# Kernel tuning notes

Measured on AMD Instinct MI355X. Metric: run time of the kernel, lower is better.

The kernel has to match this reference:

```python
import jax, jax.numpy as jnp
import numpy as np

B, V, K, DIN, H, DH, OBS, HID = 2048, 3, 32, 256, 8, 64, 128, 256
REP = H * DH
EPS = 1e-6


def _ln(x, g, b):
    mu = x.mean(-1, keepdims=True)
    var = ((x - mu) ** 2).mean(-1, keepdims=True)
    return (x - mu) * jax.lax.rsqrt(var + 1e-5) * g + b


def setup_inputs() -> dict:
    key = jax.random.key(0)
    ks = iter(jax.random.split(key, 32))
    nrm = lambda shape, s=0.05: jax.random.normal(next(ks), shape, jnp.float32) * s
    return {
        'x_anchor': jax.random.normal(next(ks), (B, V, DIN), jnp.float32),
        'x_neighbors': jax.random.normal(next(ks), (B, V, K, DIN), jnp.float32),
        'edge_weights': jax.random.uniform(next(ks), (B, V, K), jnp.float32),
        'g': jax.random.normal(next(ks), (B, OBS), jnp.float32),
        'aW': nrm((V, DIN, REP)), 'ab': jnp.zeros((V, REP)), 'ag': jnp.ones((V, REP)), 'abeta': jnp.zeros((V, REP)),
        'nW': nrm((V, DIN, REP)), 'nb': jnp.zeros((V, REP)), 'ng': jnp.ones((V, REP)), 'nbeta': jnp.zeros((V, REP)),
        'Wq': nrm((V, H, DH, DH)), 'Wk': nrm((V, H, DH, DH)), 'Wv': nrm((V, H, DH, DH)), 'Wo': nrm((V, H, DH, DH)),
        'geom_log_scale': jnp.zeros((V, H)),
        'cWq': nrm((H, DH, DH)), 'cWk': nrm((H, DH, DH)), 'cWv': nrm((H, DH, DH)), 'cWo': nrm((H, DH, DH)),
        'rW1': nrm((OBS, HID)), 'rb1': jnp.zeros((HID,)),
        'rW2': nrm((HID, HID)), 'rb2': jnp.zeros((HID,)),
        'vW': nrm((HID, H * V)), 'vb': jnp.zeros((H * V,)),
        'mW': nrm((HID, H)), 'mb': jnp.zeros((H,)),
        'gW': nrm((HID, H)), 'gb': jnp.zeros((H,)),
    }


def reference(x_anchor, x_neighbors, edge_weights, g, aW, ab, ag, abeta, nW, nb, ng, nbeta,
              Wq, Wk, Wv, Wo, geom_log_scale, cWq, cWk, cWv, cWo,
              rW1, rb1, rW2, rb2, vW, vb, mW, mb, gW, gb):
    # --- per-view encoders (vectorized over V with a leading v axis) ---
    ha = _ln(jnp.einsum('bvi,vio->bvo', x_anchor, aW) + ab, ag, abeta).reshape(B, V, H, DH)
    hn = _ln(jnp.einsum('bvki,vio->bvko', x_neighbors, nW) + nb[:, None, :],
             ng[:, None, :], nbeta[:, None, :]).reshape(B, V, K, H, DH)
    q = jnp.einsum('bvhd,vhde->bvhe', ha, Wq)
    k = jnp.einsum('bvkhd,vhde->bvkhe', hn, Wk)
    vv = jnp.einsum('bvkhd,vhde->bvkhe', hn, Wv)
    sc = jnp.einsum('bvhd,bvkhd->bvhk', q, k) / np.sqrt(DH).astype(np.float32)
    geom = jax.nn.softplus(geom_log_scale)  # [V,H]
    sc = sc + geom[None, :, :, None] * jnp.log(edge_weights[:, :, None, :] + EPS)
    attn = jax.nn.softmax(sc, axis=-1)
    ho = jnp.einsum('bvhk,bvkhd->bvhd', attn, vv)
    ho = jnp.einsum('bvhd,vhde->bvhe', ho, Wo) + ha  # residual
    view_tokens = jnp.transpose(ho, (0, 2, 1, 3))  # [B,H,V,Dh]
    # --- router ---
    hid = jax.nn.gelu(jnp.dot(g, rW1) + rb1, approximate=False)
    hid = jax.nn.gelu(jnp.dot(hid, rW2) + rb2, approximate=False)
    pi = jax.nn.softmax((jnp.dot(hid, vW) + vb).reshape(B, H, V), axis=-1)
    beta = jax.nn.sigmoid((jnp.dot(hid, mW) + mb)[..., None])  # [B,H,1]
    gate = jax.nn.softmax(jnp.dot(hid, gW) + gb, axis=-1)      # [B,H]
    # --- pi-weighted mixture + cross-view interaction with log-pi prior ---
    mix = jnp.einsum('bhv,bhvd->bhd', pi, view_tokens)
    qc = jnp.einsum('bhd,hde->bhe', mix, cWq)
    kc = jnp.einsum('bhvd,hde->bhve', view_tokens, cWk)
    vc = jnp.einsum('bhvd,hde->bhve', view_tokens, cWv)
    s2 = jnp.einsum('bhd,bhvd->bhv', qc, kc) / np.sqrt(DH).astype(np.float32) + jnp.log(pi + EPS)
    a2 = jax.nn.softmax(s2, axis=-1)
    cr = jnp.einsum('bhv,bhvd->bhd', a2, vc)
    cr = jnp.einsum('bhd,hde->bhe', cr, cWo)
    # mode blend + head gating; head_repr kept unflattened [B,H,Dh]
    return gate[..., None] * (beta * cr + (1.0 - beta) * mix)
```

## Files before the change

### kernel.cpp

```cpp
#include <hip/hip_runtime.h>

#define B_   2048
#define V_   3
#define K_   32
#define DIN_ 256
#define H_   8
#define DH_  64
#define REP_ 512

typedef unsigned short u16;
typedef unsigned int   u32;
typedef __bf16 bf8 __attribute__((ext_vector_type(8)));
typedef float  f4  __attribute__((ext_vector_type(4)));

static __device__ __forceinline__ u16 f2bf(float f) {
  union { float f; u32 i; } x; x.f = f;
  u32 r = (x.i + 0x7FFFu + ((x.i >> 16) & 1u)) >> 16;
  return (u16)r;
}
static __device__ __forceinline__ float bf2f(u16 u) {
  union { u32 i; float f; } x; x.i = ((u32)u) << 16;
  return x.f;
}
static __device__ __forceinline__ float bflo(u32 q) {
  union { u32 i; float f; } x; x.i = q << 16; return x.f;
}
static __device__ __forceinline__ float bfhi(u32 q) {
  union { u32 i; float f; } x; x.i = q & 0xffff0000u; return x.f;
}

static __device__ __forceinline__ void gl2lds16(const u16* g, u16* l) {
  __builtin_amdgcn_global_load_lds(
      (const __attribute__((address_space(1))) unsigned int*)(g),
      (__attribute__((address_space(3))) unsigned int*)(l), 16, 0, 0);
}

__global__ __launch_bounds__(256) void k0_prep(
    const float* __restrict__ nW, const float* __restrict__ aW,
    const float* __restrict__ Wv,
    u16* __restrict__ nWt, u16* __restrict__ aWt,
    u16* __restrict__ Wvt)
{
  int id = blockIdx.x * 256 + threadIdx.x;
  if (id < 393216) {
    int v  = id / 131072, r  = id % 131072;
    int kt = r / 16384,   r2 = r % 16384;
    int n  = r2 >> 5;
    int s  = (r2 >> 3) & 3;
    int m  = r2 & 7;
    int c  = s ^ ((n >> 1) & 3);
    int k  = kt * 32 + c * 8 + m;
    int src = (v * 256 + k) * 512 + n;
    nWt[id] = f2bf(nW[src]);
    aWt[id] = f2bf(aW[src]);
  } else {
    int j = id - 393216;
    int vh = j / 4096, r = j % 4096;
    int e = r / 64, d = r % 64;
    int src = (vh * 64 + d) * 64 + e;
    Wvt[j] = f2bf(Wv[src]);
  }
}

__global__ __launch_bounds__(256) void k0_wqk(
    const float* __restrict__ Wq, const float* __restrict__ Wk,
    float* __restrict__ Wqk)
{
  int vh = blockIdx.x, t = threadIdx.x;
  __shared__ float wq[4096], wkT[4096];
  #pragma unroll
  for (int i = 0; i < 16; ++i) {
    int idx = i * 256 + t;
    wq[idx] = Wq[(long)vh * 4096 + idx];
    int e = idx >> 6, c = idx & 63;
    wkT[c * 64 + e] = Wk[(long)vh * 4096 + e * 64 + c];
  }
  __syncthreads();
  int d = t >> 2, e0 = (t & 3) * 16;
  float acc[16];
  #pragma unroll
  for (int j = 0; j < 16; ++j) acc[j] = 0.f;
  for (int c = 0; c < 64; ++c) {
    float a = wq[d * 64 + c];
    const float* wr = &wkT[c * 64 + e0];
    #pragma unroll
    for (int j = 0; j < 16; ++j) acc[j] += a * wr[j];
  }
  #pragma unroll
  for (int j = 0; j < 16; ++j) Wqk[(long)vh * 4096 + d * 64 + e0 + j] = acc[j];
}

__global__ __launch_bounds__(256) void k_tq(
    const float* __restrict__ ha, const float* __restrict__ Wqk,
    float* __restrict__ tB)
{
  __shared__ float hs[512];
  int bv = blockIdx.x, t = threadIdx.x;
  int v = bv % 3;
  hs[t]       = ha[(long)bv * 512 + t];
  hs[256 + t] = ha[(long)bv * 512 + 256 + t];
  __syncthreads();
  int h = t >> 5, e0 = (t & 31) * 2;
  const float* wq = Wqk + ((long)v * 8 + h) * 4096 + e0;
  const float* hv = &hs[h * 64];
  float a0 = 0.f, a1 = 0.f;
  #pragma unroll 4
  for (int d = 0; d < 64; ++d) {
    float x = hv[d];
    float2 wv = *(const float2*)&wq[d * 64];
    a0 += x * wv.x;
    a1 += x * wv.y;
  }
  tB[(long)bv * 512 + h * 64 + e0]     = a0 * 0.125f;
  tB[(long)bv * 512 + h * 64 + e0 + 1] = a1 * 0.125f;
}

union K1Smem {
  struct { u16 A[64 * 256]; u16 B[16384]; } p;
  u16 S[64 * 512];
};

__global__ __launch_bounds__(512, 4) void k1_gemm_ln(
    const float* __restrict__ X,
    const u16*   __restrict__ Wt,
    const float* __restrict__ bias,
    const float* __restrict__ gamma,
    const float* __restrict__ betap,
    u16*   __restrict__ hn,
    float* __restrict__ ha,
    int mode, int b0, int Bc)
{
  __shared__ K1Smem sm;
  const int v = blockIdx.y, blk = blockIdx.x, t = threadIdx.x;
  const int w = t >> 6, l = t & 63, lm = l & 15, lg = l >> 4;
  const int wm = w & 1, wn = w >> 1;

  float bcol[8];
  #pragma unroll
  for (int tn = 0; tn < 8; ++tn) bcol[tn] = bias[v * 512 + wn * 128 + tn * 16 + lm];

  {
    int row = t >> 3;
    int cbase = (t & 7) * 32;
    long grow;
    if (mode == 0) { int b = b0 + blk * 2 + (row >> 5); grow = ((long)(b * 3 + v) * 32 + (row & 31)) * 256; }
    else           { int b = blk * 64 + row;            grow = (long)(b * 3 + v) * 256; }
    const float4* src = (const float4*)(X + grow + cbase);
    int sw = row & 7;
    #pragma unroll
    for (int j = 0; j < 8; ++j) {
      float4 f = src[j];
      int col = cbase + j * 4;
      int c = col >> 3, m = col & 7;
      ushort4 u;
      u.x = f2bf(f.x); u.y = f2bf(f.y); u.z = f2bf(f.z); u.w = f2bf(f.w);
      *(ushort4*)&sm.p.A[row * 256 + ((c ^ sw) << 3) + m] = u;
    }
  }

  f4 acc[2][8];
  #pragma unroll
  for (int i = 0; i < 2; ++i)
    #pragma unroll
    for (int j = 0; j < 8; ++j) { f4 z = {0.f, 0.f, 0.f, 0.f}; acc[i][j] = z; }

  const u16* Wbase = Wt + (long)v * 8 * 16384;
  for (int kt = 0; kt < 8; ++kt) {
    __syncthreads();
    {
      const u16* gp = Wbase + (long)kt * 16384 + t * 8;
      u16* lp = &sm.p.B[t * 8];
      #pragma unroll
      for (int r = 0; r < 4; ++r) gl2lds16(gp + r * 4096, lp + r * 4096);
    }
    __syncthreads();
    bf8 af[2];
    #pragma unroll
    for (int tm = 0; tm < 2; ++tm) {
      int row = wm * 32 + tm * 16 + lm;
      int c = kt * 4 + lg;
      af[tm] = *(const bf8*)&sm.p.A[row * 256 + ((c ^ (row & 7)) << 3)];
    }
    #pragma unroll
    for (int tn = 0; tn < 8; ++tn) {
      int n = wn * 128 + tn * 16 + lm;
      bf8 bv = *(const bf8*)&sm.p.B[n * 32 + ((lg ^ ((n >> 1) & 3)) << 3)];
      acc[0][tn] = __builtin_amdgcn_mfma_f32_16x16x32_bf16(af[0], bv, acc[0][tn], 0, 0, 0);
      acc[1][tn] = __builtin_amdgcn_mfma_f32_16x16x32_bf16(af[1], bv, acc[1][tn], 0, 0, 0);
    }
  }
  __syncthreads();

  #pragma unroll
  for (int tm = 0; tm < 2; ++tm)
    #pragma unroll
    for (int tn = 0; tn < 8; ++tn) {
      int col = wn * 128 + tn * 16 + lm;
      int c = col >> 3, m = col & 7;
      #pragma unroll
      for (int r = 0; r < 4; ++r) {
        int row = wm * 32 + tm * 16 + lg * 4 + r;
        sm.S[row * 512 + ((c ^ (row & 7)) << 3) + m] = f2bf(acc[tm][tn][r] + bcol[tn]);
      }
    }
  __syncthreads();

  {
    int row = t >> 3, ch = t & 7, sw = row & 7;
    float s1 = 0.f, s2 = 0.f;
    #pragma unroll
    for (int j = 0; j < 8; ++j) {
      int c = j * 8 + ch;
      uint4 q = *(const uint4*)&sm.S[row * 512 + ((c ^ sw) << 3)];
      float x0 = bflo(q.x), x1 = bfhi(q.x), x2 = bflo(q.y), x3 = bfhi(q.y);
      float x4 = bflo(q.z), x5 = bfhi(q.z), x6 = bflo(q.w), x7 = bfhi(q.w);
      s1 += ((x0 + x1) + (x2 + x3)) + ((x4 + x5) + (x6 + x7));
      s2 += ((x0*x0 + x1*x1) + (x2*x2 + x3*x3)) + ((x4*x4 + x5*x5) + (x6*x6 + x7*x7));
    }
    #pragma unroll
    for (int d = 1; d < 8; d <<= 1) { s1 += __shfl_xor(s1, d, 64); s2 += __shfl_xor(s2, d, 64); }
    float mu = s1 * (1.f / 512.f);
    float var = s2 * (1.f / 512.f) - mu * mu;
    float rs = rsqrtf(var + 1e-5f);
    #pragma unroll
    for (int j = 0; j < 8; ++j) {
      int c = j * 8 + ch;
      uint4 q = *(const uint4*)&sm.S[row * 512 + ((c ^ sw) << 3)];
      int col0 = c * 8;
      float4 g0 = *(const float4*)&gamma[v * 512 + col0];
      float4 g1 = *(const float4*)&gamma[v * 512 + col0 + 4];
      float4 e0 = *(const float4*)&betap[v * 512 + col0];
      float4 e1 = *(const float4*)&betap[v * 512 + col0 + 4];
      float y0 = (bflo(q.x) - mu) * rs * g0.x + e0.x;
      float y1 = (bfhi(q.x) - mu) * rs * g0.y + e0.y;
      float y2 = (bflo(q.y) - mu) * rs * g0.z + e0.z;
      float y3 = (bfhi(q.y) - mu) * rs * g0.w + e0.w;
      float y4 = (bflo(q.z) - mu) * rs * g1.x + e1.x;
      float y5 = (bfhi(q.z) - mu) * rs * g1.y + e1.y;
      float y6 = (bflo(q.w) - mu) * rs * g1.z + e1.z;
      float y7 = (bfhi(q.w) - mu) * rs * g1.w + e1.w;
      if (mode == 0) {
        uint4 q4;
        q4.x = (u32)f2bf(y0) | ((u32)f2bf(y1) << 16);
        q4.y = (u32)f2bf(y2) | ((u32)f2bf(y3) << 16);
        q4.z = (u32)f2bf(y4) | ((u32)f2bf(y5) << 16);
        q4.w = (u32)f2bf(y6) | ((u32)f2bf(y7) << 16);
        int bl_ = blk * 2 + (row >> 5), krow = row & 31;
        u16* dst = hn + (((long)(v * 8 + j) * Bc + bl_) * 32 + krow) * 64 + ch * 8;
        *(uint4*)dst = q4;
      } else {
        int b = blk * 64 + row;
        float* dst = ha + (long)(b * 3 + v) * 512 + col0;
        float4 w0, w1;
        w0.x = y0; w0.y = y1; w0.z = y2; w0.w = y3;
        w1.x = y4; w1.y = y5; w1.z = y6; w1.w = y7;
        *(float4*)dst = w0;
        *(float4*)(dst + 4) = w1;
      }
    }
  }
}

__global__ __launch_bounds__(512, 4) void k12_fused(
    const float* __restrict__ X,
    const u16*   __restrict__ Wt,
    const float* __restrict__ bias,
    const float* __restrict__ gamma,
    const float* __restrict__ betap,
    const float* __restrict__ ha,
    const u16*   __restrict__ Wvt,
    const float* __restrict__ tB,
    const float* __restrict__ Wo,
    const float* __restrict__ ew,
    const float* __restrict__ gls,
    float* __restrict__ vt)
{
  __shared__ K1Smem sm;
  __shared__ float tS[1024];
  __shared__ float aS[512];
  __shared__ float oSbuf[1024];
  float* lnP1 = oSbuf;
  float* lnP2 = oSbuf + 256;
  float* muRs = oSbuf + 512;

  const int v = blockIdx.y, blk = blockIdx.x, t = threadIdx.x;
  const int w = t >> 6, l = t & 63, lm = l & 15, lg = l >> 4;
  const int wm = w & 1, wn = w >> 1;

  {
    int row = t >> 3;
    int cbase = (t & 7) * 32;
    int b = blk * 2 + (row >> 5);
    long grow = ((long)(b * 3 + v) * 32 + (row & 31)) * 256;
    const float4* src = (const float4*)(X + grow + cbase);
    int sw = row & 7;
    #pragma unroll
    for (int j = 0; j < 8; ++j) {
      float4 f = src[j];
      int col = cbase + j * 4;
      int c = col >> 3, m = col & 7;
      ushort4 u;
      u.x = f2bf(f.x); u.y = f2bf(f.y); u.z = f2bf(f.z); u.w = f2bf(f.w);
      *(ushort4*)&sm.p.A[row * 256 + ((c ^ sw) << 3) + m] = u;
    }
  }
  {
    int b = t >> 8, e = (t & 255) * 2;
    *(float2*)&tS[b * 512 + e] =
        *(const float2*)&tB[((long)(blk * 2 + b) * 3 + v) * 512 + e];
  }

  f4 acc[2][8];
  #pragma unroll
  for (int i = 0; i < 2; ++i)
    #pragma unroll
    for (int j = 0; j < 8; ++j) { f4 z = {0.f, 0.f, 0.f, 0.f}; acc[i][j] = z; }

  const u16* Wbase = Wt + (long)v * 8 * 16384;
  for (int kt = 0; kt < 8; ++kt) {
    __syncthreads();
    {
      const u16* gp = Wbase + (long)kt * 16384 + t * 8;
      u16* lp = &sm.p.B[t * 8];
      #pragma unroll
      for (int r = 0; r < 4; ++r) gl2lds16(gp + r * 4096, lp + r * 4096);
    }
    __syncthreads();
    bf8 af[2];
    #pragma unroll
    for (int tm = 0; tm < 2; ++tm) {
      int row = wm * 32 + tm * 16 + lm;
      int c = kt * 4 + lg;
      af[tm] = *(const bf8*)&sm.p.A[row * 256 + ((c ^ (row & 7)) << 3)];
    }
    #pragma unroll
    for (int tn = 0; tn < 8; ++tn) {
      int n = wn * 128 + tn * 16 + lm;
      bf8 bv = *(const bf8*)&sm.p.B[n * 32 + ((lg ^ ((n >> 1) & 3)) << 3)];
      acc[0][tn] = __builtin_amdgcn_mfma_f32_16x16x32_bf16(bv, af[0], acc[0][tn], 0, 0, 0);
      acc[1][tn] = __builtin_amdgcn_mfma_f32_16x16x32_bf16(bv, af[1], acc[1][tn], 0, 0, 0);
    }
  }

  #pragma unroll
  for (int tn = 0; tn < 8; ++tn) {
    float4 bb = *(const float4*)&bias[v * 512 + wn * 128 + tn * 16 + lg * 4];
    #pragma unroll
    for (int r = 0; r < 4; ++r) { acc[0][tn][r] += ((const float*)&bb)[r]; acc[1][tn][r] += ((const float*)&bb)[r]; }
  }

  {
    #pragma unroll
    for (int tm = 0; tm < 2; ++tm) {
      float s1 = 0.f, s2 = 0.f;
      #pragma unroll
      for (int tn = 0; tn < 8; ++tn)
        #pragma unroll
        for (int r = 0; r < 4; ++r) { float z = acc[tm][tn][r]; s1 += z; s2 += z * z; }
      s1 += __shfl_xor(s1, 16, 64); s2 += __shfl_xor(s2, 16, 64);
      s1 += __shfl_xor(s1, 32, 64); s2 += __shfl_xor(s2, 32, 64);
      if (lg == 0) {
        int row = wm * 32 + tm * 16 + lm;
        lnP1[row * 4 + wn] = s1;
        lnP2[row * 4 + wn] = s2;
      }
    }
  }
  __syncthreads();
  if (t < 64) {
    float p = lnP1[t * 4] + lnP1[t * 4 + 1] + lnP1[t * 4 + 2] + lnP1[t * 4 + 3];
    float q = lnP2[t * 4] + lnP2[t * 4 + 1] + lnP2[t * 4 + 2] + lnP2[t * 4 + 3];
    float mu = p * (1.f / 512.f);
    float var = q * (1.f / 512.f) - mu * mu;
    muRs[t]      = mu;
    muRs[64 + t] = rsqrtf(var + 1e-5f);
  }
  __syncthreads();

  {
    float mu0 = muRs[wm * 32 + lm],      rs0 = muRs[64 + wm * 32 + lm];
    float mu1 = muRs[wm * 32 + 16 + lm], rs1 = muRs[64 + wm * 32 + 16 + lm];
    int row0 = wm * 32 + lm, row1 = row0 + 16;
    int sw0 = row0 & 7, sw1 = row1 & 7;
    #pragma unroll
    for (int tn = 0; tn < 8; ++tn) {
      int col0 = wn * 128 + tn * 16 + lg * 4;
      int c = col0 >> 3, m0 = col0 & 7;
      float4 g4 = *(const float4*)&gamma[v * 512 + col0];
      float4 b4 = *(const float4*)&betap[v * 512 + col0];
      {
        float y0 = (acc[0][tn][0] - mu0) * rs0 * g4.x + b4.x;
        float y1 = (acc[0][tn][1] - mu0) * rs0 * g4.y + b4.y;
        float y2 = (acc[0][tn][2] - mu0) * rs0 * g4.z + b4.z;
        float y3 = (acc[0][tn][3] - mu0) * rs0 * g4.w + b4.w;
        uint2 p;
        p.x = (u32)f2bf(y0) | ((u32)f2bf(y1) << 16);
        p.y = (u32)f2bf(y2) | ((u32)f2bf(y3) << 16);
        *(uint2*)&sm.S[row0 * 512 + ((c ^ sw0) << 3) + m0] = p;
      }
      {
        float y0 = (acc[1][tn][0] - mu1) * rs1 * g4.x + b4.x;
        float y1 = (acc[1][tn][1] - mu1) * rs1 * g4.y + b4.y;
        float y2 = (acc[1][tn][2] - mu1) * rs1 * g4.z + b4.z;
        float y3 = (acc[1][tn][3] - mu1) * rs1 * g4.w + b4.w;
        uint2 p;
        p.x = (u32)f2bf(y0) | ((u32)f2bf(y1) << 16);
        p.y = (u32)f2bf(y2) | ((u32)f2bf(y3) << 16);
        *(uint2*)&sm.S[row1 * 512 + ((c ^ sw1) << 3) + m0] = p;
      }
    }
  }
  __syncthreads();

  {
    int b = t >> 8, h = (t >> 5) & 7, k = t & 31;
    float x = gls[v * 8 + h];
    float gsc = (x > 20.f) ? x : log1pf(expf(x));
    int r = b * 32 + k, sw = r & 7;
    const float* tb = &tS[(b * 8 + h) * 64];
    float s = 0.f;
    #pragma unroll
    for (int j = 0; j < 8; ++j) {
      int c8 = h * 8 + j;
      uint4 q = *(const uint4*)&sm.S[r * 512 + ((c8 ^ sw) << 3)];
      const float* tj = tb + j * 8;
      s += tj[0] * bflo(q.x) + tj[1] * bfhi(q.x)
         + tj[2] * bflo(q.y) + tj[3] * bfhi(q.y)
         + tj[4] * bflo(q.z) + tj[5] * bfhi(q.z)
         + tj[6] * bflo(q.w) + tj[7] * bfhi(q.w);
    }
    float e_w = ew[((long)(blk * 2 + b) * 3 + v) * 32 + k];
    s += gsc * logf(e_w + 1e-6f);
    float m = s;
    #pragma unroll
    for (int d = 1; d < 32; d <<= 1) m = fmaxf(m, __shfl_xor(m, d, 64));
    float exs = expf(s - m), sum = exs;
    #pragma unroll
    for (int d = 1; d < 32; d <<= 1) sum += __shfl_xor(sum, d, 64);
    aS[(b * 8 + h) * 32 + k] = exs / sum;
  }
// ... 34 lines not shown
        int k = tm * 16 + lg * 4 + r4;
        float a = aS[p * 32 + k];
        #pragma unroll
        for (int tn = 0; tn < 4; ++tn) pp[tn] += a * aV[tm][tn][r4];
      }
    #pragma unroll
    for (int tn = 0; tn < 4; ++tn) {
      float x = pp[tn];
      x += __shfl_xor(x, 16, 64);
      x += __shfl_xor(x, 32, 64);
      if (l < 16) oSbuf[p * 64 + tn * 16 + lm] = x;
    }
  }
  __syncthreads();

  {
    int h = t >> 6, e = t & 63;
    const float* wo = Wo + (long)(v * 8 + h) * 4096;
    float a0 = ha[((long)(blk * 2 + 0) * 3 + v) * 512 + h * 64 + e];
    float a1 = ha[((long)(blk * 2 + 1) * 3 + v) * 512 + h * 64 + e];
    const float* o0 = &oSbuf[h * 64];
    const float* o1 = &oSbuf[512 + h * 64];
    #pragma unroll 8
    for (int d = 0; d < 64; ++d) {
      float wv = wo[d * 64 + e];
      a0 += o0[d] * wv;
      a1 += o1[d] * wv;
    }
    vt[(((long)(blk * 2 + 0) * 8 + h) * 3 + v) * 64 + e] = a0;
    vt[(((long)(blk * 2 + 1) * 8 + h) * 3 + v) * 64 + e] = a1;
  }
}

__global__ __launch_bounds__(256) void k3_router(
    const float* __restrict__ g, const float* __restrict__ rW1, const float* __restrict__ rb1,
    const float* __restrict__ rW2, const float* __restrict__ rb2,
    const float* __restrict__ vW, const float* __restrict__ vb,
    const float* __restrict__ mW, const float* __restrict__ mb,
    const float* __restrict__ gW, const float* __restrict__ gb,
    float* __restrict__ pi, float* __restrict__ beta_o, float* __restrict__ gate_o)
{
  __shared__ float gs[4 * 128], h1[4 * 256], h2[4 * 256], lgt[4 * 40];
  int t = threadIdx.x, bb = blockIdx.x * 4;
  #pragma unroll
  for (int r = 0; r < 2; ++r) { int idx = r * 256 + t; gs[idx] = g[(long)bb * 128 + idx]; }
  __syncthreads();
  {
    int bl = t >> 6, e0 = (t & 63) * 4;
    float acc[4];
    #pragma unroll
    for (int j = 0; j < 4; ++j) acc[j] = rb1[e0 + j];
    for (int i = 0; i < 128; ++i) {
      float gv = gs[bl * 128 + i];
      const float* wr = rW1 + i * 256 + e0;
      #pragma unroll
      for (int j = 0; j < 4; ++j) acc[j] += gv * wr[j];
    }
    #pragma unroll
    for (int j = 0; j < 4; ++j) { float x = acc[j]; h1[bl * 256 + e0 + j] = 0.5f * x * (1.f + erff(x * 0.70710678118f)); }
  }
  __syncthreads();
  {
    int bl = t >> 6, e0 = (t & 63) * 4;
    float acc[4];
    #pragma unroll
    for (int j = 0; j < 4; ++j) acc[j] = rb2[e0 + j];
    for (int i = 0; i < 256; ++i) {
      float hv = h1[bl * 256 + i];
      const float* wr = rW2 + i * 256 + e0;
      #pragma unroll
      for (int j = 0; j < 4; ++j) acc[j] += hv * wr[j];
    }
    #pragma unroll
    for (int j = 0; j < 4; ++j) { float x = acc[j]; h2[bl * 256 + e0 + j] = 0.5f * x * (1.f + erff(x * 0.70710678118f)); }
  }
  __syncthreads();
  if (t < 160) {
    int bl = t / 40, j = t % 40;
    const float* W; float bs; int col, stride;
    if (j < 24)      { W = vW; col = j;      stride = 24; bs = vb[j]; }
    else if (j < 32) { W = mW; col = j - 24; stride = 8;  bs = mb[j - 24]; }
    else             { W = gW; col = j - 32; stride = 8;  bs = gb[j - 32]; }
    float acc = bs;
    for (int i = 0; i < 256; ++i) acc += h2[bl * 256 + i] * W[i * stride + col];
    lgt[bl * 40 + j] = acc;
  }
  __syncthreads();
  if (t < 4) {
    int b = bb + t;
    const float* L = &lgt[t * 40];
    #pragma unroll
    for (int hh = 0; hh < 8; ++hh) {
      float a0 = L[hh * 3], a1 = L[hh * 3 + 1], a2v = L[hh * 3 + 2];
      float m = fmaxf(a0, fmaxf(a1, a2v));
      float x0 = expf(a0 - m), x1 = expf(a1 - m), x2 = expf(a2v - m);
      float inv = 1.f / (x0 + x1 + x2);
      pi[b * 24 + hh * 3 + 0] = x0 * inv;
      pi[b * 24 + hh * 3 + 1] = x1 * inv;
      pi[b * 24 + hh * 3 + 2] = x2 * inv;
      beta_o[b * 8 + hh] = 1.f / (1.f + expf(-L[24 + hh]));
    }
    float m = L[32];
    #pragma unroll
    for (int hh = 1; hh < 8; ++hh) m = fmaxf(m, L[32 + hh]);
    float s = 0.f, ex[8];
    #pragma unroll
    for (int hh = 0; hh < 8; ++hh) { ex[hh] = expf(L[32 + hh] - m); s += ex[hh]; }
    float inv = 1.f / s;
    #pragma unroll
    for (int hh = 0; hh < 8; ++hh) gate_o[b * 8 + hh] = ex[hh] * inv;
  }
}

__global__ __launch_bounds__(256) void k4_cross(
    const float* __restrict__ vtg, const float* __restrict__ pig,
    const float* __restrict__ betag, const float* __restrict__ gateg,
    const float* __restrict__ cWq, const float* __restrict__ cWk,
    const float* __restrict__ cWv, const float* __restrict__ cWo,
    float* __restrict__ out)
{
  __shared__ float smem[12544];
  float* vts   = smem;
  float* mixs  = smem + 6144;
  float* buf1  = smem + 8192;
  float* buf2  = smem + 10240;
  float* a2s   = smem + 12288;
  float* pis   = smem + 12384;
  float* betas = smem + 12480;
  float* gates = smem + 12512;

  int t = threadIdx.x, bblk = blockIdx.x * 4;
  {
    const float4* src = (const float4*)(vtg + (long)bblk * 1536);
    #pragma unroll
    for (int r = 0; r < 6; ++r) ((float4*)vts)[r * 256 + t] = src[r * 256 + t];
    if (t < 96) pis[t] = pig[bblk * 24 + t];
    if (t < 32) { betas[t] = betag[bblk * 8 + t]; gates[t] = gateg[bblk * 8 + t]; }
  }
  __syncthreads();
  int bl = t >> 6, hh = (t >> 3) & 7, e0 = (t & 7) * 8;
  const float* vbh = &vts[(bl * 8 + hh) * 192];
  {
    float p0 = pis[bl * 24 + hh * 3], p1 = pis[bl * 24 + hh * 3 + 1], p2 = pis[bl * 24 + hh * 3 + 2];
    #pragma unroll
    for (int j = 0; j < 8; ++j) {
      int e = e0 + j;
      mixs[(bl * 8 + hh) * 64 + e] = p0 * vbh[e] + p1 * vbh[64 + e] + p2 * vbh[128 + e];
    }
  }
  __syncthreads();
  {
    float acc[8] = {0.f,0.f,0.f,0.f,0.f,0.f,0.f,0.f};
    const float* M = &mixs[(bl * 8 + hh) * 64];
    for (int d = 0; d < 64; ++d) {
      float mv = M[d];
      const float* wr = &cWq[(hh * 64 + d) * 64 + e0];
      #pragma unroll
      for (int j = 0; j < 8; ++j) acc[j] += mv * wr[j];
    }
    #pragma unroll
    for (int j = 0; j < 8; ++j) buf1[(bl * 8 + hh) * 64 + e0 + j] = acc[j] * 0.125f;
  }
  __syncthreads();
  {
    const float* Q = &buf1[(bl * 8 + hh) * 64];
    #pragma unroll
    for (int d2 = 0; d2 < 8; ++d2) {
      const float* wr = &cWk[(hh * 64 + e0 + d2) * 64];
      float a = 0.f;
      for (int e = 0; e < 64; ++e) a += wr[e] * Q[e];
      buf2[(bl * 8 + hh) * 64 + e0 + d2] = a;
    }
// ... 23 lines not shown
    #pragma unroll
    for (int j = 0; j < 8; ++j) {
      int e = e0 + j;
      buf1[(bl * 8 + hh) * 64 + e] = a0 * vbh[e] + a1 * vbh[64 + e] + a2v * vbh[128 + e];
    }
  }
  __syncthreads();
  {
    float acc[8] = {0.f,0.f,0.f,0.f,0.f,0.f,0.f,0.f};
    const float* Y = &buf1[(bl * 8 + hh) * 64];
    for (int d = 0; d < 64; ++d) {
      float yv = Y[d];
      const float* wr = &cWv[(hh * 64 + d) * 64 + e0];
      #pragma unroll
      for (int j = 0; j < 8; ++j) acc[j] += yv * wr[j];
    }
    #pragma unroll
    for (int j = 0; j < 8; ++j) buf2[(bl * 8 + hh) * 64 + e0 + j] = acc[j];
  }
  __syncthreads();
  {
    float acc[8] = {0.f,0.f,0.f,0.f,0.f,0.f,0.f,0.f};
    const float* C2 = &buf2[(bl * 8 + hh) * 64];
    for (int d = 0; d < 64; ++d) {
      float cv = C2[d];
      const float* wr = &cWo[(hh * 64 + d) * 64 + e0];
      #pragma unroll
      for (int j = 0; j < 8; ++j) acc[j] += cv * wr[j];
    }
    float bt = betas[bl * 8 + hh], gt = gates[bl * 8 + hh];
    const float* M = &mixs[(bl * 8 + hh) * 64];
    #pragma unroll
    for (int j = 0; j < 8; ++j)
      out[((long)(bblk + bl) * 8 + hh) * 64 + e0 + j] = gt * (bt * acc[j] + (1.f - bt) * M[e0 + j]);
  }
}

extern "C" void kernel_launch(void* const* d_in, const int* in_sizes, int n_in,
                              void* d_out, int out_size, void* d_ws, size_t ws_size,
                              hipStream_t stream) {
  const float* x_anchor    = (const float*)d_in[0];
  const float* x_neighbors = (const float*)d_in[1];
  const float* edge_w      = (const float*)d_in[2];
  const float* g           = (const float*)d_in[3];
  const float* aW  = (const float*)d_in[4];
  const float* ab  = (const float*)d_in[5];
  const float* ag  = (const float*)d_in[6];
  const float* abeta = (const float*)d_in[7];
  const float* nW  = (const float*)d_in[8];
  const float* nb  = (const float*)d_in[9];
  const float* ng  = (const float*)d_in[10];
  const float* nbeta = (const float*)d_in[11];
  const float* Wq  = (const float*)d_in[12];
  const float* Wk  = (const float*)d_in[13];
  const float* Wv  = (const float*)d_in[14];
  const float* Wo  = (const float*)d_in[15];
  const float* gls = (const float*)d_in[16];
  const float* cWq = (const float*)d_in[17];
  const float* cWk = (const float*)d_in[18];
  const float* cWv = (const float*)d_in[19];
  const float* cWo = (const float*)d_in[20];
  const float* rW1 = (const float*)d_in[21];
  const float* rb1 = (const float*)d_in[22];
  const float* rW2 = (const float*)d_in[23];
  const float* rb2 = (const float*)d_in[24];
  const float* vW  = (const float*)d_in[25];
  const float* vb  = (const float*)d_in[26];
  const float* mW  = (const float*)d_in[27];
  const float* mb  = (const float*)d_in[28];
  const float* gW  = (const float*)d_in[29];
  const float* gb  = (const float*)d_in[30];

  char* p = (char*)d_ws;
  u16* nWt = (u16*)p;  p += 786432;
  u16* aWt = (u16*)p;  p += 786432;
  u16* Wvt = (u16*)p;  p += 196608;
  float* WqkB = (float*)p; p += 393216;
  float* ha   = (float*)p; p += 12582912;
  float* vtb  = (float*)p; p += 12582912;
  float* tqB  = (float*)p; p += 12582912;
  float* pib  = (float*)p; p += 196608;
  float* betb = (float*)p; p += 65536;
  float* gatb = (float*)p; p += 65536;
  (void)ws_size;

  k0_prep<<<1920, 256, 0, stream>>>(nW, aW, Wv, nWt, aWt, Wvt);
  k0_wqk<<<24, 256, 0, stream>>>(Wq, Wk, WqkB);
  k1_gemm_ln<<<dim3(32, 3), 512, 0, stream>>>(x_anchor, aWt, ab, ag, abeta,
                                              (u16*)nullptr, ha, 1, 0, 2048);
  k_tq<<<6144, 256, 0, stream>>>(ha, WqkB, tqB);
  k3_router<<<512, 256, 0, stream>>>(g, rW1, rb1, rW2, rb2, vW, vb, mW, mb, gW, gb,
                                     pib, betb, gatb);
  k12_fused<<<dim3(1024, 3), 512, 0, stream>>>(x_neighbors, nWt, nb, ng, nbeta,
                                               ha, Wvt, tqB, Wo, edge_w, gls, vtb);
  k4_cross<<<512, 256, 0, stream>>>(vtb, pib, betb, gatb, cWq, cWk, cWv, cWo,
                                    (float*)d_out);
}
```

Measured before the change: 732.2 us.

## Load GEMM weights directly to registers, fuse prep and router/cross kernels

Reorders the bf16 weight layout so each lane's MFMA B fragment is contiguous in global memory, then loads it straight into registers and drops the LDS staging and the per-k-step barriers in both GEMM kernels. The anchor GEMM now does its LayerNorm from registers instead of via a bf16 LDS round-trip. The weight-prep and Wqk kernels are merged into one launch, and so are the router and cross-view kernels, which also removes the pi/beta/gate global buffers. Float-to-bf16 conversion switches to the packed hardware instruction. The risks are exposed global-load latency inside the MFMA loop and more register pressure.

```diff
diff --git a/kernel.cpp b/kernel.cpp
--- a/kernel.cpp
+++ b/kernel.cpp
@@ -18,76 +18,64 @@
   u32 r = (x.i + 0x7FFFu + ((x.i >> 16) & 1u)) >> 16;
   return (u16)r;
 }
-static __device__ __forceinline__ float bf2f(u16 u) {
-  union { u32 i; float f; } x; x.i = ((u32)u) << 16;
-  return x.f;
-}
 static __device__ __forceinline__ float bflo(u32 q) {
   union { u32 i; float f; } x; x.i = q << 16; return x.f;
 }
 static __device__ __forceinline__ float bfhi(u32 q) {
   union { u32 i; float f; } x; x.i = q & 0xffff0000u; return x.f;
 }
-
-static __device__ __forceinline__ void gl2lds16(const u16* g, u16* l) {
-  __builtin_amdgcn_global_load_lds(
-      (const __attribute__((address_space(1))) unsigned int*)(g),
-      (__attribute__((address_space(3))) unsigned int*)(l), 16, 0, 0);
-}
-
-__global__ __launch_bounds__(256) void k0_prep(
+static __device__ __forceinline__ u32 pk2bf(float lo, float hi) {
+  u32 r;
+  asm("v_cvt_pk_bf16_f32 %0, %1, %2" : "=v"(r) : "v"(lo), "v"(hi));
+  return r;
+}
+
+__global__ __launch_bounds__(256) void k0_fuse(
     const float* __restrict__ nW, const float* __restrict__ aW,
     const float* __restrict__ Wv,
-    u16* __restrict__ nWt, u16* __restrict__ aWt,
-    u16* __restrict__ Wvt)
-{
-  int id = blockIdx.x * 256 + threadIdx.x;
-  if (id < 393216) {
-    int v  = id / 131072, r  = id % 131072;
-    int kt = r / 16384,   r2 = r % 16384;
-    int n  = r2 >> 5;
-    int s  = (r2 >> 3) & 3;
-    int m  = r2 & 7;
-    int c  = s ^ ((n >> 1) & 3);
-    int k  = kt * 32 + c * 8 + m;
-    int src = (v * 256 + k) * 512 + n;
-    nWt[id] = f2bf(nW[src]);
-    aWt[id] = f2bf(aW[src]);
-  } else {
-    int j = id - 393216;
-    int vh = j / 4096, r = j % 4096;
-    int e = r / 64, d = r % 64;
-    int src = (vh * 64 + d) * 64 + e;
-    Wvt[j] = f2bf(Wv[src]);
-  }
-}
-
-__global__ __launch_bounds__(256) void k0_wqk(
     const float* __restrict__ Wq, const float* __restrict__ Wk,
+    u16* __restrict__ nWt, u16* __restrict__ aWt, u16* __restrict__ Wvt,
     float* __restrict__ Wqk)
 {
-  int vh = blockIdx.x, t = threadIdx.x;
-  __shared__ float wq[4096], wkT[4096];
-  #pragma unroll
-  for (int i = 0; i < 16; ++i) {
-    int idx = i * 256 + t;
-    wq[idx] = Wq[(long)vh * 4096 + idx];
-    int e = idx >> 6, c = idx & 63;
-    wkT[c * 64 + e] = Wk[(long)vh * 4096 + e * 64 + c];
-  }
-  __syncthreads();
-  int d = t >> 2, e0 = (t & 3) * 16;
-  float acc[16];
-  #pragma unroll
-  for (int j = 0; j < 16; ++j) acc[j] = 0.f;
-  for (int c = 0; c < 64; ++c) {
-    float a = wq[d * 64 + c];
-    const float* wr = &wkT[c * 64 + e0];
-    #pragma unroll
-    for (int j = 0; j < 16; ++j) acc[j] += a * wr[j];
-  }
-  #pragma unroll
-  for (int j = 0; j < 16; ++j) Wqk[(long)vh * 4096 + d * 64 + e0 + j] = acc[j];
+  __shared__ float sm8[8192];
+  int bid = blockIdx.x, t = threadIdx.x;
+  if (bid < 1536) {
+    int id = bid * 256 + t;
+    int n = id & 511, k = (id >> 9) & 255, v = id >> 17;
+    int kt = k >> 5, k5 = k & 31;
+    int dst = ((v * 8 + kt) * 512 + n) * 32 + k5;
+    nWt[dst] = f2bf(nW[id]);
+    aWt[dst] = f2bf(aW[id]);
+  } else if (bid < 1920) {
+    int j = (bid - 1536) * 256 + t;
+    int vh = j >> 12, r = j & 4095;
+    int e = r >> 6, d = r & 63;
+    Wvt[j] = f2bf(Wv[(vh * 64 + d) * 64 + e]);
+  } else {
+    int vh = bid - 1920;
+    float* wq = sm8;
+    float* wkT = sm8 + 4096;
+    #pragma unroll
+    for (int i = 0; i < 16; ++i) {
+      int idx = i * 256 + t;
+      wq[idx] = Wq[(long)vh * 4096 + idx];
+      int e = idx >> 6, c = idx & 63;
+      wkT[c * 64 + e] = Wk[(long)vh * 4096 + e * 64 + c];
+    }
+    __syncthreads();
+    int d = t >> 2, e0 = (t & 3) * 16;
+    float acc[16];
+    #pragma unroll
+    for (int j = 0; j < 16; ++j) acc[j] = 0.f;
+    for (int c = 0; c < 64; ++c) {
+      float a = wq[d * 64 + c];
+      const float* wr = &wkT[c * 64 + e0];
+      #pragma unroll
+      for (int j = 0; j < 16; ++j) acc[j] += a * wr[j];
+    }
+    #pragma unroll
+    for (int j = 0; j < 16; ++j) Wqk[(long)vh * 4096 + d * 64 + e0 + j] = acc[j];
+  }
 }
 
 __global__ __launch_bounds__(256) void k_tq(
@@ -115,48 +103,39 @@
   tB[(long)bv * 512 + h * 64 + e0 + 1] = a1 * 0.125f;
 }
 
-union K1Smem {
-  struct { u16 A[64 * 256]; u16 B[16384]; } p;
-  u16 S[64 * 512];
-};
-
-__global__ __launch_bounds__(512, 4) void k1_gemm_ln(
+__global__ __launch_bounds__(512, 4) void k1a_anchor(
     const float* __restrict__ X,
     const u16*   __restrict__ Wt,
     const float* __restrict__ bias,
     const float* __restrict__ gamma,
     const float* __restrict__ betap,
-    u16*   __restrict__ hn,
-    float* __restrict__ ha,
-    int mode, int b0, int Bc)
+    float* __restrict__ ha)
 {
-  __shared__ K1Smem sm;
+  __shared__ u16 A[64 * 256];
+  __shared__ float lnP1[256], lnP2[256], muRs[128];
+
   const int v = blockIdx.y, blk = blockIdx.x, t = threadIdx.x;
   const int w = t >> 6, l = t & 63, lm = l & 15, lg = l >> 4;
   const int wm = w & 1, wn = w >> 1;
 
-  float bcol[8];
-  #pragma unroll
-  for (int tn = 0; tn < 8; ++tn) bcol[tn] = bias[v * 512 + wn * 128 + tn * 16 + lm];
-
   {
     int row = t >> 3;
     int cbase = (t & 7) * 32;
-    long grow;
-    if (mode == 0) { int b = b0 + blk * 2 + (row >> 5); grow = ((long)(b * 3 + v) * 32 + (row & 31)) * 256; }
-    else           { int b = blk * 64 + row;            grow = (long)(b * 3 + v) * 256; }
-    const float4* src = (const float4*)(X + grow + cbase);
+    int b = blk * 64 + row;
+    const float4* src = (const float4*)(X + (long)(b * 3 + v) * 256 + cbase);
     int sw = row & 7;
     #pragma unroll
     for (int j = 0; j < 8; ++j) {
       float4 f = src[j];
       int col = cbase + j * 4;
       int c = col >> 3, m = col & 7;
-      ushort4 u;
-      u.x = f2bf(f.x); u.y = f2bf(f.y); u.z = f2bf(f.z); u.w = f2bf(f.w);
-      *(ushort4*)&sm.p.A[row * 256 + ((c ^ sw) << 3) + m] = u;
-    }
-  }
+      uint2 u;
+      u.x = pk2bf(f.x, f.y);
+      u.y = pk2bf(f.z, f.w);
+      *(uint2*)&A[row * 256 + ((c ^ sw) << 3) + m] = u;
+    }
+  }
+  __syncthreads();
 
   f4 acc[2][8];
   #pragma unroll
@@ -164,102 +143,87 @@
     #pragma unroll
     for (int j = 0; j < 8; ++j) { f4 z = {0.f, 0.f, 0.f, 0.f}; acc[i][j] = z; }
 
-  const u16* Wbase = Wt + (long)v * 8 * 16384;
-  for (int kt = 0; kt < 8; ++kt) {
-    __syncthreads();
-    {
-      const u16* gp = Wbase + (long)kt * 16384 + t * 8;
-      u16* lp = &sm.p.B[t * 8];
-      #pragma unroll
-      for (int r = 0; r < 4; ++r) gl2lds16(gp + r * 4096, lp + r * 4096);
-    }
-    __syncthreads();
-    bf8 af[2];
-    #pragma unroll
-    for (int tm = 0; tm < 2; ++tm) {
+  {
+    const u16* Bv = Wt + (long)v * 131072 + ((wn * 128 + lm) * 32 + lg * 8);
+    const int row0 = wm * 32 + lm, row1 = row0 + 16;
+    #pragma unroll 1
+    for (int kt = 0; kt < 8; ++kt) {
+      const u16* bp = Bv + kt * 16384;
+      bf8 bv[8];
+      #pragma unroll
+      for (int tn = 0; tn < 8; ++tn) bv[tn] = *(const bf8*)(bp + tn * 512);
+      int c = kt * 4 + lg;
+      bf8 af0 = *(const bf8*)&A[row0 * 256 + ((c ^ (row0 & 7)) << 3)];
+      bf8 af1 = *(const bf8*)&A[row1 * 256 + ((c ^ (row1 & 7)) << 3)];
+      #pragma unroll
+      for (int tn = 0; tn < 8; ++tn) {
+        acc[0][tn] = __builtin_amdgcn_mfma_f32_16x16x32_bf16(bv[tn], af0, acc[0][tn], 0, 0, 0);
+        acc[1][tn] = __builtin_amdgcn_mfma_f32_16x16x32_bf16(bv[tn], af1, acc[1][tn], 0, 0, 0);
+      }
+    }
+  }
+
+  #pragma unroll
+  for (int tn = 0; tn < 8; ++tn) {
+    float4 bb = *(const float4*)&bias[v * 512 + wn * 128 + tn * 16 + lg * 4];
+    #pragma unroll
+    for (int r = 0; r < 4; ++r) { acc[0][tn][r] += ((const float*)&bb)[r]; acc[1][tn][r] += ((const float*)&bb)[r]; }
+  }
+
+  #pragma unroll
+  for (int tm = 0; tm < 2; ++tm) {
+    float s1 = 0.f, s2 = 0.f;
+    #pragma unroll
+    for (int tn = 0; tn < 8; ++tn)
+      #pragma unroll
+      for (int r = 0; r < 4; ++r) { float z = acc[tm][tn][r]; s1 += z; s2 += z * z; }
+    s1 += __shfl_xor(s1, 16, 64); s2 += __shfl_xor(s2, 16, 64);
+    s1 += __shfl_xor(s1, 32, 64); s2 += __shfl_xor(s2, 32, 64);
+    if (lg == 0) {
       int row = wm * 32 + tm * 16 + lm;
-      int c = kt * 4 + lg;
-      af[tm] = *(const bf8*)&sm.p.A[row * 256 + ((c ^ (row & 7)) << 3)];
-    }
+      lnP1[row * 4 + wn] = s1;
+      lnP2[row * 4 + wn] = s2;
+    }
+  }
+  __syncthreads();
+  if (t < 64) {
+    float p = lnP1[t * 4] + lnP1[t * 4 + 1] + lnP1[t * 4 + 2] + lnP1[t * 4 + 3];
+    float q = lnP2[t * 4] + lnP2[t * 4 + 1] + lnP2[t * 4 + 2] + lnP2[t * 4 + 3];
+    float mu = p * (1.f / 512.f);
+    float var = q * (1.f / 512.f) - mu * mu;
+    muRs[t]      = mu;
+    muRs[64 + t] = rsqrtf(var + 1e-5f);
+  }
+  __syncthreads();
+
+  {
+    float mu0 = muRs[wm * 32 + lm],      rs0 = muRs[64 + wm * 32 + lm];
+    float mu1 = muRs[wm * 32 + 16 + lm], rs1 = muRs[64 + wm * 32 + 16 + lm];
+    int b0g = blk * 64 + wm * 32 + lm, b1g = b0g + 16;
     #pragma unroll
     for (int tn = 0; tn < 8; ++tn) {
-      int n = wn * 128 + tn * 16 + lm;
-      bf8 bv = *(const bf8*)&sm.p.B[n * 32 + ((lg ^ ((n >> 1) & 3)) << 3)];
-      acc[0][tn] = __builtin_amdgcn_mfma_f32_16x16x32_bf16(af[0], bv, acc[0][tn], 0, 0, 0);
-      acc[1][tn] = __builtin_amdgcn_mfma_f32_16x16x32_bf16(af[1], bv, acc[1][tn], 0, 0, 0);
-    }
-  }
-  __syncthreads();
-
-  #pragma unroll
-  for (int tm = 0; tm < 2; ++tm)
-    #pragma unroll
-    for (int tn = 0; tn < 8; ++tn) {
-      int col = wn * 128 + tn * 16 + lm;
-      int c = col >> 3, m = col & 7;
-      #pragma unroll
-      for (int r = 0; r < 4; ++r) {
-        int row = wm * 32 + tm * 16 + lg * 4 + r;
-        sm.S[row * 512 + ((c ^ (row & 7)) << 3) + m] = f2bf(acc[tm][tn][r] + bcol[tn]);
-      }
-    }
-  __syncthreads();
-
-  {
-    int row = t >> 3, ch = t & 7, sw = row & 7;
-    float s1 = 0.f, s2 = 0.f;
-    #pragma unroll
-    for (int j = 0; j < 8; ++j) {
-      int c = j * 8 + ch;
-      uint4 q = *(const uint4*)&sm.S[row * 512 + ((c ^ sw) << 3)];
-      float x0 = bflo(q.x), x1 = bfhi(q.x), x2 = bflo(q.y), x3 = bfhi(q.y);
-      float x4 = bflo(q.z), x5 = bfhi(q.z), x6 = bflo(q.w), x7 = bfhi(q.w);
-      s1 += ((x0 + x1) + (x2 + x3)) + ((x4 + x5) + (x6 + x7));
-      s2 += ((x0*x0 + x1*x1) + (x2*x2 + x3*x3)) + ((x4*x4 + x5*x5) + (x6*x6 + x7*x7));
-    }
-    #pragma unroll
-    for (int d = 1; d < 8; d <<= 1) { s1 += __shfl_xor(s1, d, 64); s2 += __shfl_xor(s2, d, 64); }
-    float mu = s1 * (1.f / 512.f);
-    float var = s2 * (1.f / 512.f) - mu * mu;
-    float rs = rsqrtf(var + 1e-5f);
-    #pragma unroll
-    for (int j = 0; j < 8; ++j) {
-      int c = j * 8 + ch;
-      uint4 q = *(const uint4*)&sm.S[row * 512 + ((c ^ sw) << 3)];
-      int col0 = c * 8;
-      float4 g0 = *(const float4*)&gamma[v * 512 + col0];
-      float4 g1 = *(const float4*)&gamma[v * 512 + col0 + 4];
-      float4 e0 = *(const float4*)&betap[v * 512 + col0];
-      float4 e1 = *(const float4*)&betap[v * 512 + col0 + 4];
-      float y0 = (bflo(q.x) - mu) * rs * g0.x + e0.x;
-      float y1 = (bfhi(q.x) - mu) * rs * g0.y + e0.y;
-      float y2 = (bflo(q.y) - mu) * rs * g0.z + e0.z;
-      float y3 = (bfhi(q.y) - mu) * rs * g0.w + e0.w;
-      float y4 = (bflo(q.z) - mu) * rs * g1.x + e1.x;
-      float y5 = (bfhi(q.z) - mu) * rs * g1.y + e1.y;
-      float y6 = (bflo(q.w) - mu) * rs * g1.z + e1.z;
-      float y7 = (bfhi(q.w) - mu) * rs * g1.w + e1.w;
-      if (mode == 0) {
-        uint4 q4;
-        q4.x = (u32)f2bf(y0) | ((u32)f2bf(y1) << 16);
-        q4.y = (u32)f2bf(y2) | ((u32)f2bf(y3) << 16);
-        q4.z = (u32)f2bf(y4) | ((u32)f2bf(y5) << 16);
-        q4.w = (u32)f2bf(y6) | ((u32)f2bf(y7) << 16);
-        int bl_ = blk * 2 + (row >> 5), krow = row & 31;
-        u16* dst = hn + (((long)(v * 8 + j) * Bc + bl_) * 32 + krow) * 64 + ch * 8;
-        *(uint4*)dst = q4;
-      } else {
-        int b = blk * 64 + row;
-        float* dst = ha + (long)(b * 3 + v) * 512 + col0;
-        float4 w0, w1;
-        w0.x = y0; w0.y = y1; w0.z = y2; w0.w = y3;
-        w1.x = y4; w1.y = y5; w1.z = y6; w1.w = y7;
-        *(float4*)dst = w0;
-        *(float4*)(dst + 4) = w1;
-      }
-    }
-  }
-}
+      int col0 = wn * 128 + tn * 16 + lg * 4;
+      float4 g4 = *(const float4*)&gamma[v * 512 + col0];
+      float4 b4 = *(const float4*)&betap[v * 512 + col0];
+      float4 y;
+      y.x = (acc[0][tn][0] - mu0) * rs0 * g4.x + b4.x;
+      y.y = (acc[0][tn][1] - mu0) * rs0 * g4.y + b4.y;
+      y.z = (acc[0][tn][2] - mu0) * rs0 * g4.z + b4.z;
+      y.w = (acc[0][tn][3] - mu0) * rs0 * g4.w + b4.w;
+      *(float4*)&ha[(long)(b0g * 3 + v) * 512 + col0] = y;
+      y.x = (acc[1][tn][0] - mu1) * rs1 * g4.x + b4.x;
+      y.y = (acc[1][tn][1] - mu1) * rs1 * g4.y + b4.y;
+      y.z = (acc[1][tn][2] - mu1) * rs1 * g4.z + b4.z;
+      y.w = (acc[1][tn][3] - mu1) * rs1 * g4.w + b4.w;
+      *(float4*)&ha[(long)(b1g * 3 + v) * 512 + col0] = y;
+    }
+  }
+}
+
+union K12Smem {
+  u16 A[64 * 256];
+  u16 S[64 * 512];
+};
 
 __global__ __launch_bounds__(512, 4) void k12_fused(
     const float* __restrict__ X,
@@ -275,7 +239,7 @@
     const float* __restrict__ gls,
     float* __restrict__ vt)
 {
-  __shared__ K1Smem sm;
+  __shared__ K12Smem sm;
   __shared__ float tS[1024];
   __shared__ float aS[512];
   __shared__ float oSbuf[1024];
@@ -299,9 +263,10 @@
       float4 f = src[j];
       int col = cbase + j * 4;
       int c = col >> 3, m = col & 7;
-      ushort4 u;
-      u.x = f2bf(f.x); u.y = f2bf(f.y); u.z = f2bf(f.z); u.w = f2bf(f.w);
-      *(ushort4*)&sm.p.A[row * 256 + ((c ^ sw) << 3) + m] = u;
+      uint2 u;
+      u.x = pk2bf(f.x, f.y);
+      u.y = pk2bf(f.z, f.w);
+      *(uint2*)&sm.A[row * 256 + ((c ^ sw) << 3) + m] = u;
     }
   }
   {
@@ -309,6 +274,7 @@
     *(float2*)&tS[b * 512 + e] =
         *(const float2*)&tB[((long)(blk * 2 + b) * 3 + v) * 512 + e];
   }
+  __syncthreads();
 
   f4 acc[2][8];
   #pragma unroll
@@ -316,29 +282,23 @@
     #pragma unroll
     for (int j = 0; j < 8; ++j) { f4 z = {0.f, 0.f, 0.f, 0.f}; acc[i][j] = z; }
 
-  const u16* Wbase = Wt + (long)v * 8 * 16384;
-  for (int kt = 0; kt < 8; ++kt) {
-    __syncthreads();
-    {
-      const u16* gp = Wbase + (long)kt * 16384 + t * 8;
-      u16* lp = &sm.p.B[t * 8];
-      #pragma unroll
-      for (int r = 0; r < 4; ++r) gl2lds16(gp + r * 4096, lp + r * 4096);
-    }
-    __syncthreads();
-    bf8 af[2];
-    #pragma unroll
-    for (int tm = 0; tm < 2; ++tm) {
-      int row = wm * 32 + tm * 16 + lm;
+  {
+    const u16* Bv = Wt + (long)v * 131072 + ((wn * 128 + lm) * 32 + lg * 8);
+    const int row0 = wm * 32 + lm, row1 = row0 + 16;
+    #pragma unroll 1
+    for (int kt = 0; kt < 8; ++kt) {
+      const u16* bp = Bv + kt * 16384;
+      bf8 bv[8];
+      #pragma unroll
+      for (int tn = 0; tn < 8; ++tn) bv[tn] = *(const bf8*)(bp + tn * 512);
       int c = kt * 4 + lg;
-      af[tm] = *(const bf8*)&sm.p.A[row * 256 + ((c ^ (row & 7)) << 3)];
-    }
-    #pragma unroll
-    for (int tn = 0; tn < 8; ++tn) {
-      int n = wn * 128 + tn * 16 + lm;
-      bf8 bv = *(const bf8*)&sm.p.B[n * 32 + ((lg ^ ((n >> 1) & 3)) << 3)];
-      acc[0][tn] = __builtin_amdgcn_mfma_f32_16x16x32_bf16(bv, af[0], acc[0][tn], 0, 0, 0);
-      acc[1][tn] = __builtin_amdgcn_mfma_f32_16x16x32_bf16(bv, af[1], acc[1][tn], 0, 0, 0);
+      bf8 af0 = *(const bf8*)&sm.A[row0 * 256 + ((c ^ (row0 & 7)) << 3)];
+      bf8 af1 = *(const bf8*)&sm.A[row1 * 256 + ((c ^ (row1 & 7)) << 3)];
+      #pragma unroll
+      for (int tn = 0; tn < 8; ++tn) {
+        acc[0][tn] = __builtin_amdgcn_mfma_f32_16x16x32_bf16(bv[tn], af0, acc[0][tn], 0, 0, 0);
+        acc[1][tn] = __builtin_amdgcn_mfma_f32_16x16x32_bf16(bv[tn], af1, acc[1][tn], 0, 0, 0);
+      }
     }
   }
 
@@ -349,21 +309,19 @@
     for (int r = 0; r < 4; ++r) { acc[0][tn][r] += ((const float*)&bb)[r]; acc[1][tn][r] += ((const float*)&bb)[r]; }
   }
 
-  {
-    #pragma unroll
-    for (int tm = 0; tm < 2; ++tm) {
-      float s1 = 0.f, s2 = 0.f;
-      #pragma unroll
-      for (int tn = 0; tn < 8; ++tn)
-        #pragma unroll
-        for (int r = 0; r < 4; ++r) { float z = acc[tm][tn][r]; s1 += z; s2 += z * z; }
-      s1 += __shfl_xor(s1, 16, 64); s2 += __shfl_xor(s2, 16, 64);
-      s1 += __shfl_xor(s1, 32, 64); s2 += __shfl_xor(s2, 32, 64);
-      if (lg == 0) {
-        int row = wm * 32 + tm * 16 + lm;
-        lnP1[row * 4 + wn] = s1;
-        lnP2[row * 4 + wn] = s2;
-      }
+  #pragma unroll
+  for (int tm = 0; tm < 2; ++tm) {
+    float s1 = 0.f, s2 = 0.f;
+    #pragma unroll
+    for (int tn = 0; tn < 8; ++tn)
+      #pragma unroll
+      for (int r = 0; r < 4; ++r) { float z = acc[tm][tn][r]; s1 += z; s2 += z * z; }
+    s1 += __shfl_xor(s1, 16, 64); s2 += __shfl_xor(s2, 16, 64);
+    s1 += __shfl_xor(s1, 32, 64); s2 += __shfl_xor(s2, 32, 64);
+    if (lg == 0) {
+      int row = wm * 32 + tm * 16 + lm;
+      lnP1[row * 4 + wn] = s1;
+      lnP2[row * 4 + wn] = s2;
     }
   }
   __syncthreads();
@@ -394,8 +352,8 @@
         float y2 = (acc[0][tn][2] - mu0) * rs0 * g4.z + b4.z;
         float y3 = (acc[0][tn][3] - mu0) * rs0 * g4.w + b4.w;
         uint2 p;
-        p.x = (u32)f2bf(y0) | ((u32)f2bf(y1) << 16);
-        p.y = (u32)f2bf(y2) | ((u32)f2bf(y3) << 16);
+        p.x = pk2bf(y0, y1);
+        p.y = pk2bf(y2, y3);
         *(uint2*)&sm.S[row0 * 512 + ((c ^ sw0) << 3) + m0] = p;
       }
       {
@@ -404,8 +362,8 @@
         float y2 = (acc[1][tn][2] - mu1) * rs1 * g4.z + b4.z;
         float y3 = (acc[1][tn][3] - mu1) * rs1 * g4.w + b4.w;
         uint2 p;
-        p.x = (u32)f2bf(y0) | ((u32)f2bf(y1) << 16);
-        p.y = (u32)f2bf(y2) | ((u32)f2bf(y3) << 16);
+        p.x = pk2bf(y0, y1);
+        p.y = pk2bf(y2, y3);
         *(uint2*)&sm.S[row1 * 512 + ((c ^ sw1) << 3) + m0] = p;
       }
     }
@@ -506,19 +464,40 @@
   }
 }
 
-__global__ __launch_bounds__(256) void k3_router(
-    const float* __restrict__ g, const float* __restrict__ rW1, const float* __restrict__ rb1,
+__global__ __launch_bounds__(256) void k34_router_cross(
+    const float* __restrict__ g,
+    const float* __restrict__ rW1, const float* __restrict__ rb1,
     const float* __restrict__ rW2, const float* __restrict__ rb2,
     const float* __restrict__ vW, const float* __restrict__ vb,
     const float* __restrict__ mW, const float* __restrict__ mb,
     const float* __restrict__ gW, const float* __restrict__ gb,
-    float* __restrict__ pi, float* __restrict__ beta_o, float* __restrict__ gate_o)
+    const float* __restrict__ vtg,
+    const float* __restrict__ cWq, const float* __restrict__ cWk,
+    const float* __restrict__ cWv, const float* __restrict__ cWo,
+    float* __restrict__ out)
 {
-  __shared__ float gs[4 * 128], h1[4 * 256], h2[4 * 256], lgt[4 * 40];
+  __shared__ float smem[12544];
+  __shared__ float gs[512], h1[1024], h2[1024], lgt[160];
+  float* vts   = smem;
+  float* mixs  = smem + 6144;
+  float* buf1  = smem + 8192;
+  float* buf2  = smem + 10240;
+  float* a2s   = smem + 12288;
+  float* pis   = smem + 12384;
+  float* betas = smem + 12480;
+  float* gates = smem + 12512;
+
   int t = threadIdx.x, bb = blockIdx.x * 4;
-  #pragma unroll
-  for (int r = 0; r < 2; ++r) { int idx = r * 256 + t; gs[idx] = g[(long)bb * 128 + idx]; }
-  __syncthreads();
+
+  {
+    const float4* src = (const float4*)(vtg + (long)bb * 1536);
+    #pragma unroll
+    for (int r = 0; r < 6; ++r) ((float4*)vts)[r * 256 + t] = src[r * 256 + t];
+    gs[t]       = g[(long)bb * 128 + t];
+    gs[256 + t] = g[(long)bb * 128 + 256 + t];
+  }
+  __syncthreads();
+
   {
     int bl = t >> 6, e0 = (t & 63) * 4;
     float acc[4];
@@ -561,7 +540,6 @@
   }
   __syncthreads();
   if (t < 4) {
-    int b = bb + t;
     const float* L = &lgt[t * 40];
     #pragma unroll
     for (int hh = 0; hh < 8; ++hh) {
@@ -569,10 +547,10 @@
       float m = fmaxf(a0, fmaxf(a1, a2v));
       float x0 = expf(a0 - m), x1 = expf(a1 - m), x2 = expf(a2v - m);
       float inv = 1.f / (x0 + x1 + x2);
-      pi[b * 24 + hh * 3 + 0] = x0 * inv;
-      pi[b * 24 + hh * 3 + 1] = x1 * inv;
-      pi[b * 24 + hh * 3 + 2] = x2 * inv;
-      beta_o[b * 8 + hh] = 1.f / (1.f + expf(-L[24 + hh]));
+      pis[t * 24 + hh * 3 + 0] = x0 * inv;
+      pis[t * 24 + hh * 3 + 1] = x1 * inv;
+      pis[t * 24 + hh * 3 + 2] = x2 * inv;
+      betas[t * 8 + hh] = 1.f / (1.f + expf(-L[24 + hh]));
     }
     float m = L[32];
     #pragma unroll
@@ -582,36 +560,10 @@
     for (int hh = 0; hh < 8; ++hh) { ex[hh] = expf(L[32 + hh] - m); s += ex[hh]; }
     float inv = 1.f / s;
     #pragma unroll
-    for (int hh = 0; hh < 8; ++hh) gate_o[b * 8 + hh] = ex[hh] * inv;
-  }
-}
-
-__global__ __launch_bounds__(256) void k4_cross(
-    const float* __restrict__ vtg, const float* __restrict__ pig,
-    const float* __restrict__ betag, const float* __restrict__ gateg,
-    const float* __restrict__ cWq, const float* __restrict__ cWk,
-    const float* __restrict__ cWv, const float* __restrict__ cWo,
-    float* __restrict__ out)
-{
-  __shared__ float smem[12544];
-  float* vts   = smem;
-  float* mixs  = smem + 6144;
-  float* buf1  = smem + 8192;
-  float* buf2  = smem + 10240;
-  float* a2s   = smem + 12288;
-  float* pis   = smem + 12384;
-  float* betas = smem + 12480;
-  float* gates = smem + 12512;
-
-  int t = threadIdx.x, bblk = blockIdx.x * 4;
-  {
-    const float4* src = (const float4*)(vtg + (long)bblk * 1536);
-    #pragma unroll
-    for (int r = 0; r < 6; ++r) ((float4*)vts)[r * 256 + t] = src[r * 256 + t];
-    if (t < 96) pis[t] = pig[bblk * 24 + t];
-    if (t < 32) { betas[t] = betag[bblk * 8 + t]; gates[t] = gateg[bblk * 8 + t]; }
-  }
-  __syncthreads();
+    for (int hh = 0; hh < 8; ++hh) gates[t * 8 + hh] = ex[hh] * inv;
+  }
+  __syncthreads();
+
   int bl = t >> 6, hh = (t >> 3) & 7, e0 = (t & 7) * 8;
   const float* vbh = &vts[(bl * 8 + hh) * 192];
   {
@@ -701,7 +653,7 @@
     const float* M = &mixs[(bl * 8 + hh) * 64];
     #pragma unroll
     for (int j = 0; j < 8; ++j)
-      out[((long)(bblk + bl) * 8 + hh) * 64 + e0 + j] = gt * (bt * acc[j] + (1.f - bt) * M[e0 + j]);
+      out[((long)(bb + bl) * 8 + hh) * 64 + e0 + j] = gt * (bt * acc[j] + (1.f - bt) * M[e0 + j]);
   }
 }
 
@@ -748,20 +700,14 @@
   float* ha   = (float*)p; p += 12582912;
   float* vtb  = (float*)p; p += 12582912;
   float* tqB  = (float*)p; p += 12582912;
-  float* pib  = (float*)p; p += 196608;
-  float* betb = (float*)p; p += 65536;
-  float* gatb = (float*)p; p += 65536;
   (void)ws_size;
 
-  k0_prep<<<1920, 256, 0, stream>>>(nW, aW, Wv, nWt, aWt, Wvt);
-  k0_wqk<<<24, 256, 0, stream>>>(Wq, Wk, WqkB);
-  k1_gemm_ln<<<dim3(32, 3), 512, 0, stream>>>(x_anchor, aWt, ab, ag, abeta,
-                                              (u16*)nullptr, ha, 1, 0, 2048);
+  k0_fuse<<<1944, 256, 0, stream>>>(nW, aW, Wv, Wq, Wk, nWt, aWt, Wvt, WqkB);
+  k1a_anchor<<<dim3(32, 3), 512, 0, stream>>>(x_anchor, aWt, ab, ag, abeta, ha);
   k_tq<<<6144, 256, 0, stream>>>(ha, WqkB, tqB);
-  k3_router<<<512, 256, 0, stream>>>(g, rW1, rb1, rW2, rb2, vW, vb, mW, mb, gW, gb,
-                                     pib, betb, gatb);
   k12_fused<<<dim3(1024, 3), 512, 0, stream>>>(x_neighbors, nWt, nb, ng, nbeta,
                                                ha, Wvt, tqB, Wo, edge_w, gls, vtb);
-  k4_cross<<<512, 256, 0, stream>>>(vtb, pib, betb, gatb, cWq, cWk, cWv, cWo,
-                                    (float*)d_out);
-}
+  k34_router_cross<<<512, 256, 0, stream>>>(g, rW1, rb1, rW2, rb2, vW, vb,
+                                            mW, mb, gW, gb, vtb,
+                                            cWq, cWk, cWv, cWo, (float*)d_out);
+}
```

New measurement: 785.2 us. 7.2% more time.
